# Kernel tuning notes

Measured on AMD Instinct MI355X. Metric: run time of the kernel, lower is better.

## Reference

```python
import jax, jax.numpy as jnp
import numpy as np

B, N, D_IN, D_OUT = 16, 4096, 256, 128


def setup_inputs() -> dict:
    key = jax.random.key(0)
    ks = jax.random.split(key, 7)
    s_proj = float(np.sqrt(2.0 / D_IN))   # kaiming-ish scale
    s_mlp = float(np.sqrt(2.0 / D_OUT))
    return {
        "X": jax.random.normal(ks[0], (B, N, D_IN), dtype=jnp.float32),
        "W_proj": jax.random.normal(ks[1], (D_IN, D_OUT), dtype=jnp.float32) * s_proj,
        "b_proj": jnp.zeros((D_OUT,), dtype=jnp.float32),
        "W1": jax.random.normal(ks[2], (D_OUT, D_OUT), dtype=jnp.float32) * s_mlp,
        "b1": jnp.zeros((D_OUT,), dtype=jnp.float32),
        "W2": jax.random.normal(ks[3], (D_OUT, D_OUT), dtype=jnp.float32) * s_mlp,
        "b2": jnp.zeros((D_OUT,), dtype=jnp.float32),
    }


def reference(X, W_proj, b_proj, W1, b1, W2, b2):
    # proj: Linear(input_dim, output_dim)
    X = jnp.einsum("bnd,de->bne", X, W_proj) + b_proj
    # mlp: FeedForwardNetwork(D,D,D, num_layers=2) == Linear -> ReLU -> Linear
    X = jax.nn.relu(jnp.einsum("bnd,de->bne", X, W1) + b1)
    X = jnp.einsum("bnd,de->bne", X, W2) + b2
    # leave-one-out sum over the N axis: for each row i, sum of all rows j != i.
    # Identical math to the masked (B,N,N,D) expand-reduce in the torch source.
    return X.sum(axis=1, keepdims=True) - X
```

## Files before the change

kernel.cpp:

```cpp
#include <hip/hip_runtime.h>
#include <stdint.h>

#define D_IN  256
#define D_OUT 128
#define NSEQ  4096
#define NB    16
#define TILE_M 64
#define GRID_M ((NB * NSEQ) / TILE_M)
#define LDS_BYTES 16384

typedef __bf16 bf16x8 __attribute__((ext_vector_type(8)));
typedef float  f32x4  __attribute__((ext_vector_type(4)));

__device__ __forceinline__ unsigned short f2bf(float f) {
  union { float f; unsigned int u; } a; a.f = f;
  unsigned int r = a.u + 0x7FFFu + ((a.u >> 16) & 1u);
  return (unsigned short)(r >> 16);
}
__device__ __forceinline__ float bf2f(unsigned short u) {
  union { unsigned int u; float f; } a; a.u = ((unsigned int)u) << 16;
  return a.f;
}

__global__ __launch_bounds__(256) void prep_weights(
    const float* __restrict__ Wp, const float* __restrict__ W1, const float* __restrict__ W2,
    unsigned short* __restrict__ WpT, unsigned short* __restrict__ W1T, unsigned short* __restrict__ W2T,
    float* __restrict__ S) {
  int t = blockIdx.x * 256 + threadIdx.x;
  if (blockIdx.x == 0) {
#pragma unroll
    for (int j = 0; j < 8; ++j) S[threadIdx.x + j * 256] = 0.f;
  }
  if (t < 256 * 128) {
    int k = t >> 7, n = t & 127;
    WpT[n * 256 + k] = f2bf(Wp[t]);
  } else if (t < 256 * 128 + 128 * 128) {
    int t2 = t - 256 * 128; int k = t2 >> 7, n = t2 & 127;
    W1T[n * 128 + k] = f2bf(W1[t2]);
  } else {
    int t3 = t - 256 * 128 - 128 * 128; int k = t3 >> 7, n = t3 & 127;
    W2T[n * 128 + k] = f2bf(W2[t3]);
  }
}

template <bool USE_WS>
__global__ __launch_bounds__(256, 4) void fused3(
    const float* __restrict__ X,
    const unsigned short* __restrict__ WpT,
    const unsigned short* __restrict__ W1T,
    const unsigned short* __restrict__ W2T,
    const float* __restrict__ bproj, const float* __restrict__ b1v, const float* __restrict__ b2v,
    unsigned short* __restrict__ Y3, float* __restrict__ out, float* __restrict__ S) {
  extern __shared__ char smem[];
  unsigned short* buf0 = (unsigned short*)smem;

  const int tid  = threadIdx.x;
  const int lane = tid & 63;
  const int w    = tid >> 6;
  const int rb   = w >> 1;
  const int ch   = w & 1;
  const int q    = lane >> 4;
  const int l16  = lane & 15;
  const int rowbase = blockIdx.x * TILE_M;
  const int bidx = rowbase >> 12;

  f32x4 acc[2][4];

#pragma unroll
  for (int rt = 0; rt < 2; ++rt)
#pragma unroll
    for (int ct = 0; ct < 4; ++ct) acc[rt][ct] = (f32x4){0.f, 0.f, 0.f, 0.f};

  for (int c = 0; c < 2; ++c) {
#pragma unroll
    for (int it = 0; it < 8; ++it) {
      int i = tid + it * 256;
      int r = i >> 5, c4 = (i & 31) << 2;
      const float4 v = *(const float4*)(X + (size_t)(rowbase + r) * D_IN + c * 128 + c4);
      ushort4 u; u.x = f2bf(v.x); u.y = f2bf(v.y); u.z = f2bf(v.z); u.w = f2bf(v.w);
      *(ushort4*)(buf0 + r * 128 + ((((c4 >> 3) ^ (r & 15)) << 3) + (c4 & 7))) = u;
    }
    __syncthreads();
#pragma unroll
    for (int ks = 0; ks < 4; ++ks) {
      bf16x8 a0 = *(const bf16x8*)(buf0 + (rb * 32 + l16) * 128      + (((4 * ks + q) ^ l16) << 3));
      bf16x8 a1 = *(const bf16x8*)(buf0 + (rb * 32 + 16 + l16) * 128 + (((4 * ks + q) ^ l16) << 3));
#pragma unroll
      for (int ct = 0; ct < 4; ++ct) {
        bf16x8 b = *(const bf16x8*)(WpT + (size_t)(ch * 64 + ct * 16 + l16) * 256 + c * 128 + ks * 32 + q * 8);
        acc[0][ct] = __builtin_amdgcn_mfma_f32_16x16x32_bf16(a0, b, acc[0][ct], 0, 0, 0);
        acc[1][ct] = __builtin_amdgcn_mfma_f32_16x16x32_bf16(a1, b, acc[1][ct], 0, 0, 0);
      }
    }
    __syncthreads();
  }

#pragma unroll
  for (int ct = 0; ct < 4; ++ct) {
    const int col = ch * 64 + ct * 16 + l16;
    const float bp = bproj[col];
#pragma unroll
    for (int rt = 0; rt < 2; ++rt)
#pragma unroll
      for (int r = 0; r < 4; ++r) {
        int row = rb * 32 + rt * 16 + q * 4 + r;
        buf0[row * 128 + ((((col >> 3) ^ (row & 15)) << 3) + (col & 7))] = f2bf(acc[rt][ct][r] + bp);
      }
  }
  __syncthreads();

#pragma unroll
  for (int rt = 0; rt < 2; ++rt)
#pragma unroll
    for (int ct = 0; ct < 4; ++ct) acc[rt][ct] = (f32x4){0.f, 0.f, 0.f, 0.f};
#pragma unroll
  for (int ks = 0; ks < 4; ++ks) {
    bf16x8 a0 = *(const bf16x8*)(buf0 + (rb * 32 + l16) * 128      + (((4 * ks + q) ^ l16) << 3));
    bf16x8 a1 = *(const bf16x8*)(buf0 + (rb * 32 + 16 + l16) * 128 + (((4 * ks + q) ^ l16) << 3));
#pragma unroll
    for (int ct = 0; ct < 4; ++ct) {
      bf16x8 b = *(const bf16x8*)(W1T + (size_t)(ch * 64 + ct * 16 + l16) * 128 + ks * 32 + q * 8);
      acc[0][ct] = __builtin_amdgcn_mfma_f32_16x16x32_bf16(a0, b, acc[0][ct], 0, 0, 0);
      acc[1][ct] = __builtin_amdgcn_mfma_f32_16x16x32_bf16(a1, b, acc[1][ct], 0, 0, 0);
    }
  }
  __syncthreads();

#pragma unroll
  for (int ct = 0; ct < 4; ++ct) {
    const int col = ch * 64 + ct * 16 + l16;
    const float bb = b1v[col];
#pragma unroll
    for (int rt = 0; rt < 2; ++rt)
#pragma unroll
      for (int r = 0; r < 4; ++r) {
        int row = rb * 32 + rt * 16 + q * 4 + r;
        float v = acc[rt][ct][r] + bb;
        v = v > 0.f ? v : 0.f;
        buf0[row * 128 + ((((col >> 3) ^ (row & 15)) << 3) + (col & 7))] = f2bf(v);
      }
  }
  __syncthreads();

#pragma unroll
  for (int rt = 0; rt < 2; ++rt)
#pragma unroll
    for (int ct = 0; ct < 4; ++ct) acc[rt][ct] = (f32x4){0.f, 0.f, 0.f, 0.f};
#pragma unroll
  for (int ks = 0; ks < 4; ++ks) {
    bf16x8 a0 = *(const bf16x8*)(buf0 + (rb * 32 + l16) * 128      + (((4 * ks + q) ^ l16) << 3));
    bf16x8 a1 = *(const bf16x8*)(buf0 + (rb * 32 + 16 + l16) * 128 + (((4 * ks + q) ^ l16) << 3));
#pragma unroll
    for (int ct = 0; ct < 4; ++ct) {
      bf16x8 b = *(const bf16x8*)(W2T + (size_t)(ch * 64 + ct * 16 + l16) * 128 + ks * 32 + q * 8);
      acc[0][ct] = __builtin_amdgcn_mfma_f32_16x16x32_bf16(a0, b, acc[0][ct], 0, 0, 0);
      acc[1][ct] = __builtin_amdgcn_mfma_f32_16x16x32_bf16(a1, b, acc[1][ct], 0, 0, 0);
    }
  }
  __syncthreads();

#pragma unroll
  for (int ct = 0; ct < 4; ++ct) {
    const int col = ch * 64 + ct * 16 + l16;
    const float bb = b2v[col];
    float s = 0.f;
#pragma unroll
    for (int rt = 0; rt < 2; ++rt)
#pragma unroll
      for (int r = 0; r < 4; ++r) {
        float v = acc[rt][ct][r] + bb;
        s += v;
        int row = rb * 32 + rt * 16 + q * 4 + r;
        buf0[row * 128 + ((((col >> 3) ^ (row & 15)) << 3) + (col & 7))] = f2bf(v);
      }
    s += __shfl_down(s, 16);
    s += __shfl_down(s, 32);
    if (lane < 16) atomicAdd(S + bidx * D_OUT + col, s);
  }
  __syncthreads();

  if (USE_WS) {
#pragma unroll
    for (int it = 0; it < 4; ++it) {
      int i = tid + it * 256;
      int r = i >> 4, g = i & 15;
      *(uint4*)(Y3 + (size_t)(rowbase + r) * 128 + g * 8) =
          *(const uint4*)(buf0 + r * 128 + ((g ^ (r & 15)) << 3));
    }
  } else {
#pragma unroll
    for (int it = 0; it < 8; ++it) {
      int i = tid + it * 256;
      int r = i >> 5, c4 = (i & 31) << 2;
      ushort4 u = *(const ushort4*)(buf0 + r * 128 + ((((c4 >> 3) ^ (r & 15)) << 3) + (c4 & 7)));
      float4 v; v.x = bf2f(u.x); v.y = bf2f(u.y); v.z = bf2f(u.z); v.w = bf2f(u.w);
      *(float4*)(out + (size_t)(rowbase + r) * D_OUT + c4) = v;
    }
  }
}

__global__ __launch_bounds__(256) void finalize_ws(
    float* __restrict__ out, const unsigned short* __restrict__ Y3, const float* __restrict__ S) {
  size_t g = (size_t)blockIdx.x * 256 + threadIdx.x;
  size_t base = g * 8;
  int row = (int)(base >> 7);
  int col = (int)(base & 127);
  int b = row >> 12;
  uint4 u = *(const uint4*)(Y3 + base);
  float4 s0 = *(const float4*)(S + (b << 7) + col);
  float4 s1 = *(const float4*)(S + (b << 7) + col + 4);
  union { unsigned int u; float f; } t;
  float4 o0, o1;
  t.u = u.x << 16;          o0.x = s0.x - t.f;
  t.u = u.x & 0xFFFF0000u;  o0.y = s0.y - t.f;
  t.u = u.y << 16;          o0.z = s0.z - t.f;
  t.u = u.y & 0xFFFF0000u;  o0.w = s0.w - t.f;
  t.u = u.z << 16;          o1.x = s1.x - t.f;
  t.u = u.z & 0xFFFF0000u;  o1.y = s1.y - t.f;
  t.u = u.w << 16;          o1.z = s1.z - t.f;
  t.u = u.w & 0xFFFF0000u;  o1.w = s1.w - t.f;
  *(float4*)(out + base) = o0;
  *(float4*)(out + base + 4) = o1;
}

__global__ __launch_bounds__(256) void finalize_ip(float* __restrict__ out, const float* __restrict__ S) {
  size_t g = (size_t)blockIdx.x * 256 + threadIdx.x;
  size_t base = g * 8;
  int row = (int)(base >> 7);
  int col = (int)(base & 127);
  int b = row >> 12;
  float4 s0 = *(const float4*)(S + (b << 7) + col);
  float4 s1 = *(const float4*)(S + (b << 7) + col + 4);
  float4 y0 = *(const float4*)(out + base);
  float4 y1 = *(const float4*)(out + base + 4);
  float4 o0, o1;
  o0.x = s0.x - y0.x; o0.y = s0.y - y0.y; o0.z = s0.z - y0.z; o0.w = s0.w - y0.w;
  o1.x = s1.x - y1.x; o1.y = s1.y - y1.y; o1.z = s1.z - y1.z; o1.w = s1.w - y1.w;
  *(float4*)(out + base) = o0;
  *(float4*)(out + base + 4) = o1;
}

extern "C" void kernel_launch(void* const* d_in, const int* in_sizes, int n_in,
                              void* d_out, int out_size, void* d_ws, size_t ws_size,
                              hipStream_t stream) {
  const float* X  = (const float*)d_in[0];
  const float* Wp = (const float*)d_in[1];
  const float* bp = (const float*)d_in[2];
  const float* W1 = (const float*)d_in[3];
  const float* b1 = (const float*)d_in[4];
  const float* W2 = (const float*)d_in[5];
  const float* b2 = (const float*)d_in[6];
  float* out = (float*)d_out;

  char* ws = (char*)d_ws;
  float* S = (float*)ws;
  unsigned short* WpT = (unsigned short*)(ws + 8192);
  unsigned short* W1T = (unsigned short*)(ws + 8192 + 65536);
  unsigned short* W2T = (unsigned short*)(ws + 8192 + 65536 + 32768);
  unsigned short* Y3  = (unsigned short*)(ws + 8192 + 131072);

  const size_t need = 8192 + 131072 + (size_t)NB * NSEQ * D_OUT * 2;
  const bool use_ws = ws_size >= need;

  prep_weights<<<256, 256, 0, stream>>>(Wp, W1, W2, WpT, W1T, W2T, S);

  const int fin_blocks = (NB * NSEQ * D_OUT) / (8 * 256);
  if (use_ws) {
    fused3<true><<<GRID_M, 256, LDS_BYTES, stream>>>(X, WpT, W1T, W2T, bp, b1, b2, Y3, out, S);
    finalize_ws<<<fin_blocks, 256, 0, stream>>>(out, Y3, S);
  } else {
    fused3<false><<<GRID_M, 256, LDS_BYTES, stream>>>(X, WpT, W1T, W2T, bp, b1, b2, Y3, out, S);
    finalize_ip<<<fin_blocks, 256, 0, stream>>>(out, S);
  }
}
```

Before: 147.8 us.

## Hold weight fragments in registers per wave and replace atomics with partial-sum reduction

Each wave now owns 32 output columns across all 64 rows, so its weight fragments for each layer are loaded once into registers and prefetched during the previous stage, rather than re-read from global memory for every k-step. The per-block column sums are written to a partials buffer and summed by a new small reduction kernel, replacing global atomicAdd and the zeroing of S. Occupancy hint drops from 4 to 3 blocks per CU to fit the extra registers. This adds a kernel launch and a larger workspace, and fewer resident waves may hide latency less well.

```diff
diff --git a/kernel.cpp b/kernel.cpp
--- a/kernel.cpp
+++ b/kernel.cpp
@@ -24,13 +24,8 @@
 
 __global__ __launch_bounds__(256) void prep_weights(
     const float* __restrict__ Wp, const float* __restrict__ W1, const float* __restrict__ W2,
-    unsigned short* __restrict__ WpT, unsigned short* __restrict__ W1T, unsigned short* __restrict__ W2T,
-    float* __restrict__ S) {
+    unsigned short* __restrict__ WpT, unsigned short* __restrict__ W1T, unsigned short* __restrict__ W2T) {
   int t = blockIdx.x * 256 + threadIdx.x;
-  if (blockIdx.x == 0) {
-#pragma unroll
-    for (int j = 0; j < 8; ++j) S[threadIdx.x + j * 256] = 0.f;
-  }
   if (t < 256 * 128) {
     int k = t >> 7, n = t & 127;
     WpT[n * 256 + k] = f2bf(Wp[t]);
@@ -44,138 +39,182 @@
 }
 
 template <bool USE_WS>
-__global__ __launch_bounds__(256, 4) void fused3(
+__global__ __launch_bounds__(256, 3) void fused3(
     const float* __restrict__ X,
     const unsigned short* __restrict__ WpT,
     const unsigned short* __restrict__ W1T,
     const unsigned short* __restrict__ W2T,
     const float* __restrict__ bproj, const float* __restrict__ b1v, const float* __restrict__ b2v,
-    unsigned short* __restrict__ Y3, float* __restrict__ out, float* __restrict__ S) {
+    unsigned short* __restrict__ Y3, float* __restrict__ out, float* __restrict__ P) {
   extern __shared__ char smem[];
   unsigned short* buf0 = (unsigned short*)smem;
 
   const int tid  = threadIdx.x;
   const int lane = tid & 63;
   const int w    = tid >> 6;
-  const int rb   = w >> 1;
-  const int ch   = w & 1;
   const int q    = lane >> 4;
   const int l16  = lane & 15;
   const int rowbase = blockIdx.x * TILE_M;
-  const int bidx = rowbase >> 12;
-
-  f32x4 acc[2][4];
-
-#pragma unroll
-  for (int rt = 0; rt < 2; ++rt)
-#pragma unroll
-    for (int ct = 0; ct < 4; ++ct) acc[rt][ct] = (f32x4){0.f, 0.f, 0.f, 0.f};
-
-  for (int c = 0; c < 2; ++c) {
-#pragma unroll
-    for (int it = 0; it < 8; ++it) {
-      int i = tid + it * 256;
-      int r = i >> 5, c4 = (i & 31) << 2;
-      const float4 v = *(const float4*)(X + (size_t)(rowbase + r) * D_IN + c * 128 + c4);
-      ushort4 u; u.x = f2bf(v.x); u.y = f2bf(v.y); u.z = f2bf(v.z); u.w = f2bf(v.w);
-      *(ushort4*)(buf0 + r * 128 + ((((c4 >> 3) ^ (r & 15)) << 3) + (c4 & 7))) = u;
-    }
-    __syncthreads();
-#pragma unroll
-    for (int ks = 0; ks < 4; ++ks) {
-      bf16x8 a0 = *(const bf16x8*)(buf0 + (rb * 32 + l16) * 128      + (((4 * ks + q) ^ l16) << 3));
-      bf16x8 a1 = *(const bf16x8*)(buf0 + (rb * 32 + 16 + l16) * 128 + (((4 * ks + q) ^ l16) << 3));
-#pragma unroll
-      for (int ct = 0; ct < 4; ++ct) {
-        bf16x8 b = *(const bf16x8*)(WpT + (size_t)(ch * 64 + ct * 16 + l16) * 256 + c * 128 + ks * 32 + q * 8);
-        acc[0][ct] = __builtin_amdgcn_mfma_f32_16x16x32_bf16(a0, b, acc[0][ct], 0, 0, 0);
-        acc[1][ct] = __builtin_amdgcn_mfma_f32_16x16x32_bf16(a1, b, acc[1][ct], 0, 0, 0);
+
+  const int col0 = w * 32 + l16;
+  const int col1 = col0 + 16;
+
+  f32x4 acc[4][2];
+  bf16x8 bA[8], bB[8];
+
+#pragma unroll
+  for (int ks = 0; ks < 4; ++ks) {
+    bA[ks * 2 + 0] = *(const bf16x8*)(WpT + (size_t)col0 * 256 + ks * 32 + q * 8);
+    bA[ks * 2 + 1] = *(const bf16x8*)(WpT + (size_t)col1 * 256 + ks * 32 + q * 8);
+  }
+
+#pragma unroll
+  for (int it = 0; it < 8; ++it) {
+    int i = tid + it * 256;
+    int r = i >> 5, c4 = (i & 31) << 2;
+    const float4 v = *(const float4*)(X + (size_t)(rowbase + r) * D_IN + c4);
+    ushort4 u; u.x = f2bf(v.x); u.y = f2bf(v.y); u.z = f2bf(v.z); u.w = f2bf(v.w);
+    *(ushort4*)(buf0 + r * 128 + ((((c4 >> 3) ^ (r & 15)) << 3) + (c4 & 7))) = u;
+  }
+
+#pragma unroll
+  for (int rt = 0; rt < 4; ++rt)
+#pragma unroll
+    for (int ct = 0; ct < 2; ++ct) acc[rt][ct] = (f32x4){0.f, 0.f, 0.f, 0.f};
+
+  __syncthreads();
+
+#pragma unroll
+  for (int ks = 0; ks < 4; ++ks) {
+    bB[ks * 2 + 0] = *(const bf16x8*)(WpT + (size_t)col0 * 256 + 128 + ks * 32 + q * 8);
+    bB[ks * 2 + 1] = *(const bf16x8*)(WpT + (size_t)col1 * 256 + 128 + ks * 32 + q * 8);
+  }
+
+#pragma unroll
+  for (int ks = 0; ks < 4; ++ks) {
+#pragma unroll
+    for (int rt = 0; rt < 4; ++rt) {
+      bf16x8 a = *(const bf16x8*)(buf0 + (rt * 16 + l16) * 128 + (((4 * ks + q) ^ l16) << 3));
+      acc[rt][0] = __builtin_amdgcn_mfma_f32_16x16x32_bf16(a, bA[ks * 2 + 0], acc[rt][0], 0, 0, 0);
+      acc[rt][1] = __builtin_amdgcn_mfma_f32_16x16x32_bf16(a, bA[ks * 2 + 1], acc[rt][1], 0, 0, 0);
+    }
+  }
+  __syncthreads();
+
+#pragma unroll
+  for (int it = 0; it < 8; ++it) {
+    int i = tid + it * 256;
+    int r = i >> 5, c4 = (i & 31) << 2;
+    const float4 v = *(const float4*)(X + (size_t)(rowbase + r) * D_IN + 128 + c4);
+    ushort4 u; u.x = f2bf(v.x); u.y = f2bf(v.y); u.z = f2bf(v.z); u.w = f2bf(v.w);
+    *(ushort4*)(buf0 + r * 128 + ((((c4 >> 3) ^ (r & 15)) << 3) + (c4 & 7))) = u;
+  }
+  __syncthreads();
+
+#pragma unroll
+  for (int ks = 0; ks < 4; ++ks) {
+    bA[ks * 2 + 0] = *(const bf16x8*)(W1T + (size_t)col0 * 128 + ks * 32 + q * 8);
+    bA[ks * 2 + 1] = *(const bf16x8*)(W1T + (size_t)col1 * 128 + ks * 32 + q * 8);
+  }
+
+#pragma unroll
+  for (int ks = 0; ks < 4; ++ks) {
+#pragma unroll
+    for (int rt = 0; rt < 4; ++rt) {
+      bf16x8 a = *(const bf16x8*)(buf0 + (rt * 16 + l16) * 128 + (((4 * ks + q) ^ l16) << 3));
+      acc[rt][0] = __builtin_amdgcn_mfma_f32_16x16x32_bf16(a, bB[ks * 2 + 0], acc[rt][0], 0, 0, 0);
+      acc[rt][1] = __builtin_amdgcn_mfma_f32_16x16x32_bf16(a, bB[ks * 2 + 1], acc[rt][1], 0, 0, 0);
+    }
+  }
+  __syncthreads();
+
+  {
+    const float bp0 = bproj[col0], bp1 = bproj[col1];
+#pragma unroll
+    for (int rt = 0; rt < 4; ++rt)
+#pragma unroll
+      for (int r = 0; r < 4; ++r) {
+        int row = rt * 16 + q * 4 + r;
+        int sw = (row & 15) << 3;
+        buf0[row * 128 + ((((col0 >> 3) << 3) ^ sw) + (col0 & 7))] = f2bf(acc[rt][0][r] + bp0);
+        buf0[row * 128 + ((((col1 >> 3) << 3) ^ sw) + (col1 & 7))] = f2bf(acc[rt][1][r] + bp1);
       }
-    }
-    __syncthreads();
-  }
-
-#pragma unroll
-  for (int ct = 0; ct < 4; ++ct) {
-    const int col = ch * 64 + ct * 16 + l16;
-    const float bp = bproj[col];
-#pragma unroll
-    for (int rt = 0; rt < 2; ++rt)
+  }
+  __syncthreads();
+
+#pragma unroll
+  for (int ks = 0; ks < 4; ++ks) {
+    bB[ks * 2 + 0] = *(const bf16x8*)(W2T + (size_t)col0 * 128 + ks * 32 + q * 8);
+    bB[ks * 2 + 1] = *(const bf16x8*)(W2T + (size_t)col1 * 128 + ks * 32 + q * 8);
+  }
+
+#pragma unroll
+  for (int rt = 0; rt < 4; ++rt)
+#pragma unroll
+    for (int ct = 0; ct < 2; ++ct) acc[rt][ct] = (f32x4){0.f, 0.f, 0.f, 0.f};
+#pragma unroll
+  for (int ks = 0; ks < 4; ++ks) {
+#pragma unroll
+    for (int rt = 0; rt < 4; ++rt) {
+      bf16x8 a = *(const bf16x8*)(buf0 + (rt * 16 + l16) * 128 + (((4 * ks + q) ^ l16) << 3));
+      acc[rt][0] = __builtin_amdgcn_mfma_f32_16x16x32_bf16(a, bA[ks * 2 + 0], acc[rt][0], 0, 0, 0);
+      acc[rt][1] = __builtin_amdgcn_mfma_f32_16x16x32_bf16(a, bA[ks * 2 + 1], acc[rt][1], 0, 0, 0);
+    }
+  }
+  __syncthreads();
+
+  {
+    const float bb0 = b1v[col0], bb1 = b1v[col1];
+#pragma unroll
+    for (int rt = 0; rt < 4; ++rt)
 #pragma unroll
       for (int r = 0; r < 4; ++r) {
-        int row = rb * 32 + rt * 16 + q * 4 + r;
-        buf0[row * 128 + ((((col >> 3) ^ (row & 15)) << 3) + (col & 7))] = f2bf(acc[rt][ct][r] + bp);
+        int row = rt * 16 + q * 4 + r;
+        int sw = (row & 15) << 3;
+        float v0 = acc[rt][0][r] + bb0; v0 = v0 > 0.f ? v0 : 0.f;
+        float v1 = acc[rt][1][r] + bb1; v1 = v1 > 0.f ? v1 : 0.f;
+        buf0[row * 128 + ((((col0 >> 3) << 3) ^ sw) + (col0 & 7))] = f2bf(v0);
+        buf0[row * 128 + ((((col1 >> 3) << 3) ^ sw) + (col1 & 7))] = f2bf(v1);
       }
   }
   __syncthreads();
 
 #pragma unroll
-  for (int rt = 0; rt < 2; ++rt)
-#pragma unroll
-    for (int ct = 0; ct < 4; ++ct) acc[rt][ct] = (f32x4){0.f, 0.f, 0.f, 0.f};
-#pragma unroll
-  for (int ks = 0; ks < 4; ++ks) {
-    bf16x8 a0 = *(const bf16x8*)(buf0 + (rb * 32 + l16) * 128      + (((4 * ks + q) ^ l16) << 3));
-    bf16x8 a1 = *(const bf16x8*)(buf0 + (rb * 32 + 16 + l16) * 128 + (((4 * ks + q) ^ l16) << 3));
-#pragma unroll
-    for (int ct = 0; ct < 4; ++ct) {
-      bf16x8 b = *(const bf16x8*)(W1T + (size_t)(ch * 64 + ct * 16 + l16) * 128 + ks * 32 + q * 8);
-      acc[0][ct] = __builtin_amdgcn_mfma_f32_16x16x32_bf16(a0, b, acc[0][ct], 0, 0, 0);
-      acc[1][ct] = __builtin_amdgcn_mfma_f32_16x16x32_bf16(a1, b, acc[1][ct], 0, 0, 0);
-    }
-  }
-  __syncthreads();
-
-#pragma unroll
-  for (int ct = 0; ct < 4; ++ct) {
-    const int col = ch * 64 + ct * 16 + l16;
-    const float bb = b1v[col];
-#pragma unroll
-    for (int rt = 0; rt < 2; ++rt)
+  for (int rt = 0; rt < 4; ++rt)
+#pragma unroll
+    for (int ct = 0; ct < 2; ++ct) acc[rt][ct] = (f32x4){0.f, 0.f, 0.f, 0.f};
+#pragma unroll
+  for (int ks = 0; ks < 4; ++ks) {
+#pragma unroll
+    for (int rt = 0; rt < 4; ++rt) {
+      bf16x8 a = *(const bf16x8*)(buf0 + (rt * 16 + l16) * 128 + (((4 * ks + q) ^ l16) << 3));
+      acc[rt][0] = __builtin_amdgcn_mfma_f32_16x16x32_bf16(a, bB[ks * 2 + 0], acc[rt][0], 0, 0, 0);
+      acc[rt][1] = __builtin_amdgcn_mfma_f32_16x16x32_bf16(a, bB[ks * 2 + 1], acc[rt][1], 0, 0, 0);
+    }
+  }
+  __syncthreads();
+
+  {
+    const float bb0 = b2v[col0], bb1 = b2v[col1];
+    float s0 = 0.f, s1 = 0.f;
+#pragma unroll
+    for (int rt = 0; rt < 4; ++rt)
 #pragma unroll
       for (int r = 0; r < 4; ++r) {
-        int row = rb * 32 + rt * 16 + q * 4 + r;
-        float v = acc[rt][ct][r] + bb;
-        v = v > 0.f ? v : 0.f;
-        buf0[row * 128 + ((((col >> 3) ^ (row & 15)) << 3) + (col & 7))] = f2bf(v);
+        int row = rt * 16 + q * 4 + r;
+        int sw = (row & 15) << 3;
+        float v0 = acc[rt][0][r] + bb0;
+        float v1 = acc[rt][1][r] + bb1;
+        s0 += v0; s1 += v1;
+        buf0[row * 128 + ((((col0 >> 3) << 3) ^ sw) + (col0 & 7))] = f2bf(v0);
+        buf0[row * 128 + ((((col1 >> 3) << 3) ^ sw) + (col1 & 7))] = f2bf(v1);
       }
-  }
-  __syncthreads();
-
-#pragma unroll
-  for (int rt = 0; rt < 2; ++rt)
-#pragma unroll
-    for (int ct = 0; ct < 4; ++ct) acc[rt][ct] = (f32x4){0.f, 0.f, 0.f, 0.f};
-#pragma unroll
-  for (int ks = 0; ks < 4; ++ks) {
-    bf16x8 a0 = *(const bf16x8*)(buf0 + (rb * 32 + l16) * 128      + (((4 * ks + q) ^ l16) << 3));
-    bf16x8 a1 = *(const bf16x8*)(buf0 + (rb * 32 + 16 + l16) * 128 + (((4 * ks + q) ^ l16) << 3));
-#pragma unroll
-    for (int ct = 0; ct < 4; ++ct) {
-      bf16x8 b = *(const bf16x8*)(W2T + (size_t)(ch * 64 + ct * 16 + l16) * 128 + ks * 32 + q * 8);
-      acc[0][ct] = __builtin_amdgcn_mfma_f32_16x16x32_bf16(a0, b, acc[0][ct], 0, 0, 0);
-      acc[1][ct] = __builtin_amdgcn_mfma_f32_16x16x32_bf16(a1, b, acc[1][ct], 0, 0, 0);
-    }
-  }
-  __syncthreads();
-
-#pragma unroll
-  for (int ct = 0; ct < 4; ++ct) {
-    const int col = ch * 64 + ct * 16 + l16;
-    const float bb = b2v[col];
-    float s = 0.f;
-#pragma unroll
-    for (int rt = 0; rt < 2; ++rt)
-#pragma unroll
-      for (int r = 0; r < 4; ++r) {
-        float v = acc[rt][ct][r] + bb;
-        s += v;
-        int row = rb * 32 + rt * 16 + q * 4 + r;
-        buf0[row * 128 + ((((col >> 3) ^ (row & 15)) << 3) + (col & 7))] = f2bf(v);
-      }
-    s += __shfl_down(s, 16);
-    s += __shfl_down(s, 32);
-    if (lane < 16) atomicAdd(S + bidx * D_OUT + col, s);
+    s0 += __shfl_down(s0, 16); s0 += __shfl_down(s0, 32);
+    s1 += __shfl_down(s1, 16); s1 += __shfl_down(s1, 32);
+    if (lane < 16) {
+      P[(size_t)blockIdx.x * 128 + col0] = s0;
+      P[(size_t)blockIdx.x * 128 + col1] = s1;
+    }
   }
   __syncthreads();
 
@@ -197,6 +236,19 @@
       *(float4*)(out + (size_t)(rowbase + r) * D_OUT + c4) = v;
     }
   }
+}
+
+__global__ __launch_bounds__(256) void reduce_S(const float* __restrict__ P, float* __restrict__ S) {
+  __shared__ float tmp[128];
+  int b = blockIdx.x;
+  int col = threadIdx.x & 127;
+  int h = threadIdx.x >> 7;
+  float s = 0.f;
+#pragma unroll
+  for (int i = 0; i < 32; ++i) s += P[(size_t)(b * 64 + h * 32 + i) * 128 + col];
+  if (h == 1) tmp[col] = s;
+  __syncthreads();
+  if (h == 0) S[b * 128 + col] = s + tmp[col];
 }
 
 __global__ __launch_bounds__(256) void finalize_ws(
@@ -257,19 +309,22 @@
   unsigned short* WpT = (unsigned short*)(ws + 8192);
   unsigned short* W1T = (unsigned short*)(ws + 8192 + 65536);
   unsigned short* W2T = (unsigned short*)(ws + 8192 + 65536 + 32768);
-  unsigned short* Y3  = (unsigned short*)(ws + 8192 + 131072);
-
-  const size_t need = 8192 + 131072 + (size_t)NB * NSEQ * D_OUT * 2;
+  float* P = (float*)(ws + 8192 + 131072);
+  unsigned short* Y3 = (unsigned short*)(ws + 8192 + 131072 + 524288);
+
+  const size_t need = 8192 + 131072 + 524288 + (size_t)NB * NSEQ * D_OUT * 2;
   const bool use_ws = ws_size >= need;
 
-  prep_weights<<<256, 256, 0, stream>>>(Wp, W1, W2, WpT, W1T, W2T, S);
+  prep_weights<<<256, 256, 0, stream>>>(Wp, W1, W2, WpT, W1T, W2T);
 
   const int fin_blocks = (NB * NSEQ * D_OUT) / (8 * 256);
   if (use_ws) {
-    fused3<true><<<GRID_M, 256, LDS_BYTES, stream>>>(X, WpT, W1T, W2T, bp, b1, b2, Y3, out, S);
+    fused3<true><<<GRID_M, 256, LDS_BYTES, stream>>>(X, WpT, W1T, W2T, bp, b1, b2, Y3, out, P);
+    reduce_S<<<NB, 256, 0, stream>>>(P, S);
     finalize_ws<<<fin_blocks, 256, 0, stream>>>(out, Y3, S);
   } else {
-    fused3<false><<<GRID_M, 256, LDS_BYTES, stream>>>(X, WpT, W1T, W2T, bp, b1, b2, Y3, out, S);
+    fused3<false><<<GRID_M, 256, LDS_BYTES, stream>>>(X, WpT, W1T, W2T, bp, b1, b2, Y3, out, P);
+    reduce_S<<<NB, 256, 0, stream>>>(P, S);
     finalize_ip<<<fin_blocks, 256, 0, stream>>>(out, S);
   }
 }
```

Result: faster. 138.4 us (-6.4%).

## Give each wave its own 16-row tile and replace atomics with partial-sum reduction

Applied to the files above, without the earlier changes.

Restructures the fused MLP kernel so each wave owns a private 16-row LDS tile (padded stride, no swizzle) and computes all 128 output columns. This removes every block-level __syncthreads. The weight B-fragments are double-buffered from global memory. The per-column atomicAdd into S is replaced by per-wave partial sums written to a workspace buffer, followed by a new reduce_S kernel, which removes the memset in prep_weights. The bf16 conversion now uses the native cast. In exchange there is an extra kernel launch and more register pressure, since launch bounds drop from 4 to 3 blocks per CU.

```diff
diff --git a/kernel.cpp b/kernel.cpp
--- a/kernel.cpp
+++ b/kernel.cpp
@@ -5,17 +5,18 @@
 #define D_OUT 128
 #define NSEQ  4096
 #define NB    16
-#define TILE_M 64
-#define GRID_M ((NB * NSEQ) / TILE_M)
-#define LDS_BYTES 16384
+#define SW    136
+#define WAVE_LDS (16 * SW)
+#define LDS_BYTES (4 * WAVE_LDS * 2)
+#define GRID_M ((NB * NSEQ) / 64)
 
 typedef __bf16 bf16x8 __attribute__((ext_vector_type(8)));
 typedef float  f32x4  __attribute__((ext_vector_type(4)));
 
 __device__ __forceinline__ unsigned short f2bf(float f) {
-  union { float f; unsigned int u; } a; a.f = f;
-  unsigned int r = a.u + 0x7FFFu + ((a.u >> 16) & 1u);
-  return (unsigned short)(r >> 16);
+  __bf16 h = (__bf16)f;
+  union { __bf16 h; unsigned short u; } c; c.h = h;
+  return c.u;
 }
 __device__ __forceinline__ float bf2f(unsigned short u) {
   union { unsigned int u; float f; } a; a.u = ((unsigned int)u) << 16;
@@ -24,13 +25,8 @@
 
 __global__ __launch_bounds__(256) void prep_weights(
     const float* __restrict__ Wp, const float* __restrict__ W1, const float* __restrict__ W2,
-    unsigned short* __restrict__ WpT, unsigned short* __restrict__ W1T, unsigned short* __restrict__ W2T,
-    float* __restrict__ S) {
+    unsigned short* __restrict__ WpT, unsigned short* __restrict__ W1T, unsigned short* __restrict__ W2T) {
   int t = blockIdx.x * 256 + threadIdx.x;
-  if (blockIdx.x == 0) {
-#pragma unroll
-    for (int j = 0; j < 8; ++j) S[threadIdx.x + j * 256] = 0.f;
-  }
   if (t < 256 * 128) {
     int k = t >> 7, n = t & 127;
     WpT[n * 256 + k] = f2bf(Wp[t]);
@@ -43,159 +39,153 @@
   }
 }
 
+__device__ __forceinline__ void gemm128(const unsigned short* __restrict__ WT,
+                                        const unsigned short* wbuf,
+                                        int l16, int q, f32x4* acc) {
+  bf16x8 bb[2][8];
+#pragma unroll
+  for (int ct = 0; ct < 8; ++ct) {
+    acc[ct] = (f32x4){0.f, 0.f, 0.f, 0.f};
+    bb[0][ct] = *(const bf16x8*)(WT + (size_t)(ct * 16 + l16) * 128 + q * 8);
+  }
+#pragma unroll
+  for (int ks = 0; ks < 4; ++ks) {
+    if (ks < 3) {
+#pragma unroll
+      for (int ct = 0; ct < 8; ++ct)
+        bb[(ks + 1) & 1][ct] = *(const bf16x8*)(WT + (size_t)(ct * 16 + l16) * 128 + (ks + 1) * 32 + q * 8);
+    }
+    bf16x8 a = *(const bf16x8*)(wbuf + l16 * SW + ks * 32 + q * 8);
+#pragma unroll
+    for (int ct = 0; ct < 8; ++ct)
+      acc[ct] = __builtin_amdgcn_mfma_f32_16x16x32_bf16(a, bb[ks & 1][ct], acc[ct], 0, 0, 0);
+  }
+}
+
 template <bool USE_WS>
-__global__ __launch_bounds__(256, 4) void fused3(
+__global__ __launch_bounds__(256, 3) void fused3(
     const float* __restrict__ X,
     const unsigned short* __restrict__ WpT,
     const unsigned short* __restrict__ W1T,
     const unsigned short* __restrict__ W2T,
     const float* __restrict__ bproj, const float* __restrict__ b1v, const float* __restrict__ b2v,
-    unsigned short* __restrict__ Y3, float* __restrict__ out, float* __restrict__ S) {
-  extern __shared__ char smem[];
-  unsigned short* buf0 = (unsigned short*)smem;
-
+    unsigned short* __restrict__ Y3, float* __restrict__ out, float* __restrict__ P) {
+  extern __shared__ unsigned short smem[];
   const int tid  = threadIdx.x;
   const int lane = tid & 63;
   const int w    = tid >> 6;
-  const int rb   = w >> 1;
-  const int ch   = w & 1;
   const int q    = lane >> 4;
   const int l16  = lane & 15;
-  const int rowbase = blockIdx.x * TILE_M;
-  const int bidx = rowbase >> 12;
-
-  f32x4 acc[2][4];
-
-#pragma unroll
-  for (int rt = 0; rt < 2; ++rt)
-#pragma unroll
-    for (int ct = 0; ct < 4; ++ct) acc[rt][ct] = (f32x4){0.f, 0.f, 0.f, 0.f};
+  unsigned short* wbuf = smem + w * WAVE_LDS;
+  const int rowbase = blockIdx.x * 64 + w * 16;
+  const int gw = blockIdx.x * 4 + w;
+
+  f32x4 acc[8];
+#pragma unroll
+  for (int ct = 0; ct < 8; ++ct) acc[ct] = (f32x4){0.f, 0.f, 0.f, 0.f};
 
   for (int c = 0; c < 2; ++c) {
 #pragma unroll
-    for (int it = 0; it < 8; ++it) {
-      int i = tid + it * 256;
-      int r = i >> 5, c4 = (i & 31) << 2;
+    for (int t = 0; t < 8; ++t) {
+      int flat4 = t * 64 + lane;
+      int r = flat4 >> 5, c4 = (flat4 & 31) << 2;
       const float4 v = *(const float4*)(X + (size_t)(rowbase + r) * D_IN + c * 128 + c4);
       ushort4 u; u.x = f2bf(v.x); u.y = f2bf(v.y); u.z = f2bf(v.z); u.w = f2bf(v.w);
-      *(ushort4*)(buf0 + r * 128 + ((((c4 >> 3) ^ (r & 15)) << 3) + (c4 & 7))) = u;
-    }
-    __syncthreads();
+      *(ushort4*)(wbuf + r * SW + c4) = u;
+    }
+    bf16x8 bb[2][8];
+#pragma unroll
+    for (int ct = 0; ct < 8; ++ct)
+      bb[0][ct] = *(const bf16x8*)(WpT + (size_t)(ct * 16 + l16) * 256 + c * 128 + q * 8);
 #pragma unroll
     for (int ks = 0; ks < 4; ++ks) {
-      bf16x8 a0 = *(const bf16x8*)(buf0 + (rb * 32 + l16) * 128      + (((4 * ks + q) ^ l16) << 3));
-      bf16x8 a1 = *(const bf16x8*)(buf0 + (rb * 32 + 16 + l16) * 128 + (((4 * ks + q) ^ l16) << 3));
-#pragma unroll
-      for (int ct = 0; ct < 4; ++ct) {
-        bf16x8 b = *(const bf16x8*)(WpT + (size_t)(ch * 64 + ct * 16 + l16) * 256 + c * 128 + ks * 32 + q * 8);
-        acc[0][ct] = __builtin_amdgcn_mfma_f32_16x16x32_bf16(a0, b, acc[0][ct], 0, 0, 0);
-        acc[1][ct] = __builtin_amdgcn_mfma_f32_16x16x32_bf16(a1, b, acc[1][ct], 0, 0, 0);
+      if (ks < 3) {
+#pragma unroll
+        for (int ct = 0; ct < 8; ++ct)
+          bb[(ks + 1) & 1][ct] = *(const bf16x8*)(WpT + (size_t)(ct * 16 + l16) * 256 + c * 128 + (ks + 1) * 32 + q * 8);
       }
-    }
-    __syncthreads();
-  }
-
-#pragma unroll
-  for (int ct = 0; ct < 4; ++ct) {
-    const int col = ch * 64 + ct * 16 + l16;
+      bf16x8 a = *(const bf16x8*)(wbuf + l16 * SW + ks * 32 + q * 8);
+#pragma unroll
+      for (int ct = 0; ct < 8; ++ct)
+        acc[ct] = __builtin_amdgcn_mfma_f32_16x16x32_bf16(a, bb[ks & 1][ct], acc[ct], 0, 0, 0);
+    }
+  }
+
+#pragma unroll
+  for (int ct = 0; ct < 8; ++ct) {
+    const int col = ct * 16 + l16;
     const float bp = bproj[col];
 #pragma unroll
-    for (int rt = 0; rt < 2; ++rt)
-#pragma unroll
-      for (int r = 0; r < 4; ++r) {
-        int row = rb * 32 + rt * 16 + q * 4 + r;
-        buf0[row * 128 + ((((col >> 3) ^ (row & 15)) << 3) + (col & 7))] = f2bf(acc[rt][ct][r] + bp);
-      }
-  }
-  __syncthreads();
-
-#pragma unroll
-  for (int rt = 0; rt < 2; ++rt)
-#pragma unroll
-    for (int ct = 0; ct < 4; ++ct) acc[rt][ct] = (f32x4){0.f, 0.f, 0.f, 0.f};
-#pragma unroll
-  for (int ks = 0; ks < 4; ++ks) {
-    bf16x8 a0 = *(const bf16x8*)(buf0 + (rb * 32 + l16) * 128      + (((4 * ks + q) ^ l16) << 3));
-    bf16x8 a1 = *(const bf16x8*)(buf0 + (rb * 32 + 16 + l16) * 128 + (((4 * ks + q) ^ l16) << 3));
-#pragma unroll
-    for (int ct = 0; ct < 4; ++ct) {
-      bf16x8 b = *(const bf16x8*)(W1T + (size_t)(ch * 64 + ct * 16 + l16) * 128 + ks * 32 + q * 8);
-      acc[0][ct] = __builtin_amdgcn_mfma_f32_16x16x32_bf16(a0, b, acc[0][ct], 0, 0, 0);
-      acc[1][ct] = __builtin_amdgcn_mfma_f32_16x16x32_bf16(a1, b, acc[1][ct], 0, 0, 0);
-    }
-  }
-  __syncthreads();
-
-#pragma unroll
-  for (int ct = 0; ct < 4; ++ct) {
-    const int col = ch * 64 + ct * 16 + l16;
-    const float bb = b1v[col];
-#pragma unroll
-    for (int rt = 0; rt < 2; ++rt)
-#pragma unroll
-      for (int r = 0; r < 4; ++r) {
-        int row = rb * 32 + rt * 16 + q * 4 + r;
-        float v = acc[rt][ct][r] + bb;
-        v = v > 0.f ? v : 0.f;
-        buf0[row * 128 + ((((col >> 3) ^ (row & 15)) << 3) + (col & 7))] = f2bf(v);
-      }
-  }
-  __syncthreads();
-
-#pragma unroll
-  for (int rt = 0; rt < 2; ++rt)
-#pragma unroll
-    for (int ct = 0; ct < 4; ++ct) acc[rt][ct] = (f32x4){0.f, 0.f, 0.f, 0.f};
-#pragma unroll
-  for (int ks = 0; ks < 4; ++ks) {
-    bf16x8 a0 = *(const bf16x8*)(buf0 + (rb * 32 + l16) * 128      + (((4 * ks + q) ^ l16) << 3));
-    bf16x8 a1 = *(const bf16x8*)(buf0 + (rb * 32 + 16 + l16) * 128 + (((4 * ks + q) ^ l16) << 3));
-#pragma unroll
-    for (int ct = 0; ct < 4; ++ct) {
-      bf16x8 b = *(const bf16x8*)(W2T + (size_t)(ch * 64 + ct * 16 + l16) * 128 + ks * 32 + q * 8);
-      acc[0][ct] = __builtin_amdgcn_mfma_f32_16x16x32_bf16(a0, b, acc[0][ct], 0, 0, 0);
-      acc[1][ct] = __builtin_amdgcn_mfma_f32_16x16x32_bf16(a1, b, acc[1][ct], 0, 0, 0);
-    }
-  }
-  __syncthreads();
-
-#pragma unroll
-  for (int ct = 0; ct < 4; ++ct) {
-    const int col = ch * 64 + ct * 16 + l16;
-    const float bb = b2v[col];
+    for (int r = 0; r < 4; ++r)
+      wbuf[(q * 4 + r) * SW + col] = f2bf(acc[ct][r] + bp);
+  }
+
+  gemm128(W1T, wbuf, l16, q, acc);
+#pragma unroll
+  for (int ct = 0; ct < 8; ++ct) {
+    const int col = ct * 16 + l16;
+    const float bb1 = b1v[col];
+#pragma unroll
+    for (int r = 0; r < 4; ++r) {
+      float v = acc[ct][r] + bb1;
+      v = v > 0.f ? v : 0.f;
+      wbuf[(q * 4 + r) * SW + col] = f2bf(v);
+    }
+  }
+
+  gemm128(W2T, wbuf, l16, q, acc);
+
+#pragma unroll
+  for (int ct = 0; ct < 8; ++ct) {
+    const int col = ct * 16 + l16;
+    const float bb2 = b2v[col];
     float s = 0.f;
 #pragma unroll
-    for (int rt = 0; rt < 2; ++rt)
-#pragma unroll
-      for (int r = 0; r < 4; ++r) {
-        float v = acc[rt][ct][r] + bb;
-        s += v;
-        int row = rb * 32 + rt * 16 + q * 4 + r;
-        buf0[row * 128 + ((((col >> 3) ^ (row & 15)) << 3) + (col & 7))] = f2bf(v);
-      }
+    for (int r = 0; r < 4; ++r) {
+      float v = acc[ct][r] + bb2;
+      s += v;
+      wbuf[(q * 4 + r) * SW + col] = f2bf(v);
+    }
     s += __shfl_down(s, 16);
     s += __shfl_down(s, 32);
-    if (lane < 16) atomicAdd(S + bidx * D_OUT + col, s);
-  }
-  __syncthreads();
+    if (lane < 16) P[(size_t)gw * 128 + col] = s;
+  }
 
   if (USE_WS) {
 #pragma unroll
     for (int it = 0; it < 4; ++it) {
-      int i = tid + it * 256;
+      int i = it * 64 + lane;
       int r = i >> 4, g = i & 15;
       *(uint4*)(Y3 + (size_t)(rowbase + r) * 128 + g * 8) =
-          *(const uint4*)(buf0 + r * 128 + ((g ^ (r & 15)) << 3));
+          *(const uint4*)(wbuf + r * SW + g * 8);
     }
   } else {
 #pragma unroll
     for (int it = 0; it < 8; ++it) {
-      int i = tid + it * 256;
-      int r = i >> 5, c4 = (i & 31) << 2;
-      ushort4 u = *(const ushort4*)(buf0 + r * 128 + ((((c4 >> 3) ^ (r & 15)) << 3) + (c4 & 7)));
+      int flat4 = it * 64 + lane;
+      int r = flat4 >> 5, c4 = (flat4 & 31) << 2;
+      ushort4 u = *(const ushort4*)(wbuf + r * SW + c4);
       float4 v; v.x = bf2f(u.x); v.y = bf2f(u.y); v.z = bf2f(u.z); v.w = bf2f(u.w);
       *(float4*)(out + (size_t)(rowbase + r) * D_OUT + c4) = v;
     }
+  }
+}
+
+__global__ __launch_bounds__(256) void reduce_S(const float* __restrict__ P, float* __restrict__ S) {
+  __shared__ float red[256];
+  int b = blockIdx.x;
+  int col = blockIdx.y * 32 + (threadIdx.x & 31);
+  int seg = threadIdx.x >> 5;
+  float s = 0.f;
+#pragma unroll
+  for (int i = 0; i < 32; ++i) s += P[(size_t)(b * 256 + seg * 32 + i) * 128 + col];
+  red[threadIdx.x] = s;
+  __syncthreads();
+  if (seg == 0) {
+    float t = s;
+#pragma unroll
+    for (int k = 1; k < 8; ++k) t += red[k * 32 + (threadIdx.x & 31)];
+    S[b * 128 + col] = t;
   }
 }
 
@@ -209,16 +199,16 @@
   uint4 u = *(const uint4*)(Y3 + base);
   float4 s0 = *(const float4*)(S + (b << 7) + col);
   float4 s1 = *(const float4*)(S + (b << 7) + col + 4);
-  union { unsigned int u; float f; } t;
+  union { unsigned int uu; float f; } t;
   float4 o0, o1;
-  t.u = u.x << 16;          o0.x = s0.x - t.f;
-  t.u = u.x & 0xFFFF0000u;  o0.y = s0.y - t.f;
-  t.u = u.y << 16;          o0.z = s0.z - t.f;
-  t.u = u.y & 0xFFFF0000u;  o0.w = s0.w - t.f;
-  t.u = u.z << 16;          o1.x = s1.x - t.f;
-  t.u = u.z & 0xFFFF0000u;  o1.y = s1.y - t.f;
-  t.u = u.w << 16;          o1.z = s1.z - t.f;
-  t.u = u.w & 0xFFFF0000u;  o1.w = s1.w - t.f;
+  t.uu = u.x << 16;          o0.x = s0.x - t.f;
+  t.uu = u.x & 0xFFFF0000u;  o0.y = s0.y - t.f;
+  t.uu = u.y << 16;          o0.z = s0.z - t.f;
+  t.uu = u.y & 0xFFFF0000u;  o0.w = s0.w - t.f;
+  t.uu = u.z << 16;          o1.x = s1.x - t.f;
+  t.uu = u.z & 0xFFFF0000u;  o1.y = s1.y - t.f;
+  t.uu = u.w << 16;          o1.z = s1.z - t.f;
+  t.uu = u.w & 0xFFFF0000u;  o1.w = s1.w - t.f;
   *(float4*)(out + base) = o0;
   *(float4*)(out + base + 4) = o1;
 }
@@ -257,19 +247,22 @@
   unsigned short* WpT = (unsigned short*)(ws + 8192);
   unsigned short* W1T = (unsigned short*)(ws + 8192 + 65536);
   unsigned short* W2T = (unsigned short*)(ws + 8192 + 65536 + 32768);
-  unsigned short* Y3  = (unsigned short*)(ws + 8192 + 131072);
-
-  const size_t need = 8192 + 131072 + (size_t)NB * NSEQ * D_OUT * 2;
+  float* P = (float*)(ws + 8192 + 131072);
+  unsigned short* Y3 = (unsigned short*)(ws + 8192 + 131072 + 2097152);
+
+  const size_t need = 8192 + 131072 + 2097152 + (size_t)NB * NSEQ * D_OUT * 2;
   const bool use_ws = ws_size >= need;
 
-  prep_weights<<<256, 256, 0, stream>>>(Wp, W1, W2, WpT, W1T, W2T, S);
+  prep_weights<<<256, 256, 0, stream>>>(Wp, W1, W2, WpT, W1T, W2T);
 
   const int fin_blocks = (NB * NSEQ * D_OUT) / (8 * 256);
   if (use_ws) {
-    fused3<true><<<GRID_M, 256, LDS_BYTES, stream>>>(X, WpT, W1T, W2T, bp, b1, b2, Y3, out, S);
+    fused3<true><<<GRID_M, 256, LDS_BYTES, stream>>>(X, WpT, W1T, W2T, bp, b1, b2, Y3, out, P);
+    reduce_S<<<dim3(NB, 4), 256, 0, stream>>>(P, S);
     finalize_ws<<<fin_blocks, 256, 0, stream>>>(out, Y3, S);
   } else {
-    fused3<false><<<GRID_M, 256, LDS_BYTES, stream>>>(X, WpT, W1T, W2T, bp, b1, b2, Y3, out, S);
+    fused3<false><<<GRID_M, 256, LDS_BYTES, stream>>>(X, WpT, W1T, W2T, bp, b1, b2, Y3, out, P);
+    reduce_S<<<dim3(NB, 4), 256, 0, stream>>>(P, S);
     finalize_ip<<<fin_blocks, 256, 0, stream>>>(out, S);
   }
 }
```

Measured after the change: 175.6 us. +18.8%, slower.
